# Optimization experiments

Measured on AMD Instinct MI355X. Metric: run time of the kernel, lower is better.

Reference implementation:

```python
import jax, jax.numpy as jnp
import numpy as np

N_RNA, N_PROT, D, C, E = 20000, 5000, 128, 4, 500000

def setup_inputs() -> dict:
    key = jax.random.key(0)
    k1, k2, k3, k4, k5, k6 = jax.random.split(key, 6)
    return {
        "RNA_inputs": jax.random.normal(k1, (N_RNA, D), dtype=jnp.float32),
        "protein_inputs": jax.random.normal(k2, (N_PROT, D), dtype=jnp.float32),
        "RNA_indices": jax.random.randint(k3, (E,), 0, N_RNA, dtype=jnp.int64),
        "protein_indices": jax.random.randint(k4, (E,), 0, N_PROT, dtype=jnp.int64),
        "w_relation": jax.random.normal(k5, (C, D), dtype=jnp.float32),
        "weight_classifier": jax.random.normal(k6, (C, C), dtype=jnp.float32),
    }

def reference(RNA_inputs, protein_inputs, RNA_indices, protein_indices, w_relation, weight_classifier):
    # Gather node features for each pair (dropout p=0.0 -> identity)
    r = RNA_inputs[RNA_indices]        # [E, D]
    p = protein_inputs[protein_indices]  # [E, D]
    # Per-class bilinear: basis[e, c] = sum_d r[e,d] * w_relation[c,d] * p[e,d]
    basis = jnp.einsum('ed,cd->ec', r * p, w_relation)  # [E, C]
    # Classifier matmul + ReLU activation
    return jax.nn.relu(basis @ weight_classifier)  # [E, C]
```

## Files before the change

kernel.cpp:

```cpp
#include <hip/hip_runtime.h>

#define DIM 128
#define NCLS 4

typedef _Float16 f16x4 __attribute__((ext_vector_type(4)));
typedef _Float16 f16x8 __attribute__((ext_vector_type(8)));

__global__ __launch_bounds__(256) void cvt_both_kernel(
    const float* __restrict__ s1, _Float16* __restrict__ d1, int n1,
    const float* __restrict__ s2, _Float16* __restrict__ d2, int n2)
{
    const int total = n1 + n2;
    int i = (blockIdx.x * blockDim.x + threadIdx.x) * 8;
    const int stride = gridDim.x * blockDim.x * 8;
    for (; i < total; i += stride) {
        const float* s; _Float16* d; int j;
        if (i < n1) { s = s1; d = d1; j = i; }
        else        { s = s2; d = d2; j = i - n1; }
        const float4 a = *(const float4*)(s + j);
        const float4 b = *(const float4*)(s + j + 4);
        f16x8 o;
        o[0] = (_Float16)a.x; o[1] = (_Float16)a.y;
        o[2] = (_Float16)a.z; o[3] = (_Float16)a.w;
        o[4] = (_Float16)b.x; o[5] = (_Float16)b.y;
        o[6] = (_Float16)b.z; o[7] = (_Float16)b.w;
        *(f16x8*)(d + j) = o;
    }
}

__device__ __forceinline__ float reduce4(float b0, float b1, float b2, float b3, int lane)
{
    const bool lo1 = (lane & 1) == 0;
    float k0 = lo1 ? b0 : b2, s0 = lo1 ? b2 : b0;
    float k1 = lo1 ? b1 : b3, s1 = lo1 ? b3 : b1;
    float v0 = k0 + __shfl_xor(s0, 1, 32);
    float v1 = k1 + __shfl_xor(s1, 1, 32);
    const bool lo2 = (lane & 2) == 0;
    float k = lo2 ? v0 : v1, s = lo2 ? v1 : v0;
    float v = k + __shfl_xor(s, 2, 32);
    v += __shfl_xor(v, 4, 32);
    v += __shfl_xor(v, 8, 32);
    v += __shfl_xor(v, 16, 32);
    return v;
}

__device__ __forceinline__ void dot_store(
    f16x4 r, f16x4 p, const float4& wf0, const float4& wf1,
    const float4& wf2, const float4& wf3, int lane, int cls,
    float* __restrict__ out, long e)
{
    const f16x4 q = r * p;
    const float qx = (float)q[0], qy = (float)q[1];
    const float qz = (float)q[2], qw = (float)q[3];
    float b0 = qx * wf0.x + qy * wf0.y + qz * wf0.z + qw * wf0.w;
    float b1 = qx * wf1.x + qy * wf1.y + qz * wf1.z + qw * wf1.w;
    float b2 = qx * wf2.x + qy * wf2.y + qz * wf2.z + qw * wf2.w;
    float b3 = qx * wf3.x + qy * wf3.y + qz * wf3.z + qw * wf3.w;
    const float v = reduce4(b0, b1, b2, b3, lane);
    if (lane < 4) out[e * NCLS + cls] = fmaxf(v, 0.0f);
}

__global__ __launch_bounds__(256, 5) void decoder_ilp8_kernel(
    const _Float16* __restrict__ rna,
    const _Float16* __restrict__ prot,
    const int*   __restrict__ ridx,
    const int*   __restrict__ pidx,
    const float* __restrict__ wrel,
    const float* __restrict__ wcls,
    float*       __restrict__ out,
    int nEdges)
{
    const int l32 = threadIdx.x & 31;
    const int hw  = (blockIdx.x * blockDim.x + threadIdx.x) >> 5;
    const int nhw = (gridDim.x * blockDim.x) >> 5;

    const float4 w0 = *(const float4*)(wrel + 0 * DIM + l32 * 4);
    const float4 w1 = *(const float4*)(wrel + 1 * DIM + l32 * 4);
    const float4 w2 = *(const float4*)(wrel + 2 * DIM + l32 * 4);
    const float4 w3 = *(const float4*)(wrel + 3 * DIM + l32 * 4);
    float wc[16];
#pragma unroll
    for (int i = 0; i < 16; ++i) wc[i] = wcls[i];
    float4 wf0, wf1, wf2, wf3;
    {
        float4* wfp[4] = {&wf0, &wf1, &wf2, &wf3};
#pragma unroll
        for (int j = 0; j < 4; ++j) {
            wfp[j]->x = wc[j] * w0.x + wc[4 + j] * w1.x + wc[8 + j] * w2.x + wc[12 + j] * w3.x;
            wfp[j]->y = wc[j] * w0.y + wc[4 + j] * w1.y + wc[8 + j] * w2.y + wc[12 + j] * w3.y;
            wfp[j]->z = wc[j] * w0.z + wc[4 + j] * w1.z + wc[8 + j] * w2.z + wc[12 + j] * w3.z;
            wfp[j]->w = wc[j] * w0.w + wc[4 + j] * w1.w + wc[8 + j] * w2.w + wc[12 + j] * w3.w;
        }
    }
    const int cls = ((l32 & 1) << 1) | ((l32 >> 1) & 1);

    const long step = (long)nhw * 8;
    long e0 = (long)hw * 8;
    if (e0 + 7 >= nEdges) return;

    int4 riA = *(const int4*)(ridx + e0);
    int4 piA = *(const int4*)(pidx + e0);
    int4 riB = *(const int4*)(ridx + e0 + 4);
    int4 piB = *(const int4*)(pidx + e0 + 4);

    for (;;) {
        const f16x4 rA0 = ((const f16x4*)(rna + (size_t)riA.x * DIM))[l32];
        const f16x4 rA1 = ((const f16x4*)(rna + (size_t)riA.y * DIM))[l32];
        const f16x4 rA2 = ((const f16x4*)(rna + (size_t)riA.z * DIM))[l32];
        const f16x4 rA3 = ((const f16x4*)(rna + (size_t)riA.w * DIM))[l32];
        const f16x4 pA0 = ((const f16x4*)(prot + (size_t)piA.x * DIM))[l32];
        const f16x4 pA1 = ((const f16x4*)(prot + (size_t)piA.y * DIM))[l32];
        const f16x4 pA2 = ((const f16x4*)(prot + (size_t)piA.z * DIM))[l32];
        const f16x4 pA3 = ((const f16x4*)(prot + (size_t)piA.w * DIM))[l32];
        const f16x4 rB0 = ((const f16x4*)(rna + (size_t)riB.x * DIM))[l32];
        const f16x4 rB1 = ((const f16x4*)(rna + (size_t)riB.y * DIM))[l32];
        const f16x4 rB2 = ((const f16x4*)(rna + (size_t)riB.z * DIM))[l32];
        const f16x4 rB3 = ((const f16x4*)(rna + (size_t)riB.w * DIM))[l32];
        const f16x4 pB0 = ((const f16x4*)(prot + (size_t)piB.x * DIM))[l32];
        const f16x4 pB1 = ((const f16x4*)(prot + (size_t)piB.y * DIM))[l32];
        const f16x4 pB2 = ((const f16x4*)(prot + (size_t)piB.z * DIM))[l32];
        const f16x4 pB3 = ((const f16x4*)(prot + (size_t)piB.w * DIM))[l32];

        const long en = e0 + step;
        const bool more = (en + 7) < nEdges;
        if (more) {
            riA = *(const int4*)(ridx + en);
            piA = *(const int4*)(pidx + en);
            riB = *(const int4*)(ridx + en + 4);
            piB = *(const int4*)(pidx + en + 4);
        }

        dot_store(rA0, pA0, wf0, wf1, wf2, wf3, l32, cls, out, e0 + 0);
        dot_store(rA1, pA1, wf0, wf1, wf2, wf3, l32, cls, out, e0 + 1);
        dot_store(rA2, pA2, wf0, wf1, wf2, wf3, l32, cls, out, e0 + 2);
        dot_store(rA3, pA3, wf0, wf1, wf2, wf3, l32, cls, out, e0 + 3);
        dot_store(rB0, pB0, wf0, wf1, wf2, wf3, l32, cls, out, e0 + 4);
        dot_store(rB1, pB1, wf0, wf1, wf2, wf3, l32, cls, out, e0 + 5);
        dot_store(rB2, pB2, wf0, wf1, wf2, wf3, l32, cls, out, e0 + 6);
        dot_store(rB3, pB3, wf0, wf1, wf2, wf3, l32, cls, out, e0 + 7);

        if (!more) break;
        e0 = en;
    }
}

__global__ __launch_bounds__(256) void decoder_f32_kernel(
    const float* __restrict__ rna, const float* __restrict__ prot,
    const int* __restrict__ ridx, const int* __restrict__ pidx,
    const float* __restrict__ wrel, const float* __restrict__ wcls,
    float* __restrict__ out, int nEdges)
{
    const int lane32 = threadIdx.x & 31;
    const int hw     = (blockIdx.x * blockDim.x + threadIdx.x) >> 5;
    const int nhw    = (gridDim.x * blockDim.x) >> 5;
    const float4 w0 = *(const float4*)(wrel + 0 * DIM + lane32 * 4);
    const float4 w1 = *(const float4*)(wrel + 1 * DIM + lane32 * 4);
    const float4 w2 = *(const float4*)(wrel + 2 * DIM + lane32 * 4);
    const float4 w3 = *(const float4*)(wrel + 3 * DIM + lane32 * 4);
    float wc[16];
#pragma unroll
    for (int i = 0; i < 16; ++i) wc[i] = wcls[i];
    float4 wf[4];
#pragma unroll
    for (int j = 0; j < 4; ++j) {
        wf[j].x = wc[j] * w0.x + wc[4 + j] * w1.x + wc[8 + j] * w2.x + wc[12 + j] * w3.x;
        wf[j].y = wc[j] * w0.y + wc[4 + j] * w1.y + wc[8 + j] * w2.y + wc[12 + j] * w3.y;
        wf[j].z = wc[j] * w0.z + wc[4 + j] * w1.z + wc[8 + j] * w2.z + wc[12 + j] * w3.z;
        wf[j].w = wc[j] * w0.w + wc[4 + j] * w1.w + wc[8 + j] * w2.w + wc[12 + j] * w3.w;
    }
    const int cls   = ((lane32 & 1) << 1) | ((lane32 >> 1) & 1);
    const int lelem = lane32 * 4;
    for (int e = hw; e < nEdges; e += nhw) {
        const float4 r = *(const float4*)(rna  + (size_t)ridx[e] * DIM + lelem);
        const float4 p = *(const float4*)(prot + (size_t)pidx[e] * DIM + lelem);
        float qx = r.x * p.x, qy = r.y * p.y, qz = r.z * p.z, qw = r.w * p.w;
        float b0 = qx * wf[0].x + qy * wf[0].y + qz * wf[0].z + qw * wf[0].w;
        float b1 = qx * wf[1].x + qy * wf[1].y + qz * wf[1].z + qw * wf[1].w;
        float b2 = qx * wf[2].x + qy * wf[2].y + qz * wf[2].z + qw * wf[2].w;
        float b3 = qx * wf[3].x + qy * wf[3].y + qz * wf[3].z + qw * wf[3].w;
        const float v = reduce4(b0, b1, b2, b3, lane32);
        if (lane32 < 4) out[(size_t)e * NCLS + cls] = fmaxf(v, 0.0f);
    }
}

extern "C" void kernel_launch(void* const* d_in, const int* in_sizes, int n_in,
                              void* d_out, int out_size, void* d_ws, size_t ws_size,
                              hipStream_t stream) {
    const float* rna  = (const float*)d_in[0];
    const float* prot = (const float*)d_in[1];
    const int*   ridx = (const int*)d_in[2];
    const int*   pidx = (const int*)d_in[3];
    const float* wrel = (const float*)d_in[4];
    const float* wcls = (const float*)d_in[5];
    float*       out  = (float*)d_out;

    const int nRnaElems  = in_sizes[0];
    const int nProtElems = in_sizes[1];
    const int nEdges     = in_sizes[2];

    const size_t rnaBytes  = (size_t)nRnaElems * 2;
    const size_t needBytes = rnaBytes + (size_t)nProtElems * 2;

    if (ws_size >= needBytes && (nEdges % 8) == 0 && nEdges >= 8 &&
        (nRnaElems % 8) == 0 && (nProtElems % 8) == 0) {
        _Float16* rnaH  = (_Float16*)d_ws;
        _Float16* protH = (_Float16*)((char*)d_ws + rnaBytes);

        const int totalElems = nRnaElems + nProtElems;
        const int cvtBlocks  = (totalElems / 8 + 255) / 256;
        hipLaunchKernelGGL(cvt_both_kernel, dim3(cvtBlocks), dim3(256), 0, stream,
                           rna, rnaH, nRnaElems, prot, protH, nProtElems);

        hipLaunchKernelGGL(decoder_ilp8_kernel, dim3(2048), dim3(256), 0, stream,
                           rnaH, protH, ridx, pidx, wrel, wcls, out, nEdges);
    } else {
        hipLaunchKernelGGL(decoder_f32_kernel, dim3(8192), dim3(256), 0, stream,
                           rna, prot, ridx, pidx, wrel, wcls, out, nEdges);
    }
}
```

Before: 105.2 us.

## Raise per-halfwave ILP to 12 edges and use fp16 dot2 for class projections

Each 32-lane group now gathers 12 edges per iteration instead of 8, using clamped overlapping groups of 4 to handle tails. The per-edge class dot products use packed fp16 dot2 instructions, with the combined weights kept in fp16. The occupancy hint drops from 5 to 4 to make room for the extra registers. The aim is more memory-level parallelism on the random gathers and fewer ALU ops, at the cost of lower occupancy, some redundant tail writes and reduced weight precision.

```diff
diff --git a/kernel.cpp b/kernel.cpp
--- a/kernel.cpp
+++ b/kernel.cpp
@@ -3,6 +3,7 @@
 #define DIM 128
 #define NCLS 4
 
+typedef _Float16 f16x2 __attribute__((ext_vector_type(2)));
 typedef _Float16 f16x4 __attribute__((ext_vector_type(4)));
 typedef _Float16 f16x8 __attribute__((ext_vector_type(8)));
 
@@ -45,22 +46,21 @@
 }
 
 __device__ __forceinline__ void dot_store(
-    f16x4 r, f16x4 p, const float4& wf0, const float4& wf1,
-    const float4& wf2, const float4& wf3, int lane, int cls,
-    float* __restrict__ out, long e)
+    f16x4 r, f16x4 p, const f16x2 (&wl)[4], const f16x2 (&wh)[4],
+    int lane, int cls, float* __restrict__ out, int e)
 {
     const f16x4 q = r * p;
-    const float qx = (float)q[0], qy = (float)q[1];
-    const float qz = (float)q[2], qw = (float)q[3];
-    float b0 = qx * wf0.x + qy * wf0.y + qz * wf0.z + qw * wf0.w;
-    float b1 = qx * wf1.x + qy * wf1.y + qz * wf1.z + qw * wf1.w;
-    float b2 = qx * wf2.x + qy * wf2.y + qz * wf2.z + qw * wf2.w;
-    float b3 = qx * wf3.x + qy * wf3.y + qz * wf3.z + qw * wf3.w;
+    const f16x2 ql = {q[0], q[1]};
+    const f16x2 qh = {q[2], q[3]};
+    const float b0 = __builtin_amdgcn_fdot2(ql, wl[0], __builtin_amdgcn_fdot2(qh, wh[0], 0.0f, false), false);
+    const float b1 = __builtin_amdgcn_fdot2(ql, wl[1], __builtin_amdgcn_fdot2(qh, wh[1], 0.0f, false), false);
+    const float b2 = __builtin_amdgcn_fdot2(ql, wl[2], __builtin_amdgcn_fdot2(qh, wh[2], 0.0f, false), false);
+    const float b3 = __builtin_amdgcn_fdot2(ql, wl[3], __builtin_amdgcn_fdot2(qh, wh[3], 0.0f, false), false);
     const float v = reduce4(b0, b1, b2, b3, lane);
-    if (lane < 4) out[e * NCLS + cls] = fmaxf(v, 0.0f);
-}
-
-__global__ __launch_bounds__(256, 5) void decoder_ilp8_kernel(
+    if (lane < 4) out[(size_t)e * NCLS + cls] = fmaxf(v, 0.0f);
+}
+
+__global__ __launch_bounds__(256, 4) void decoder_ilp12_kernel(
     const _Float16* __restrict__ rna,
     const _Float16* __restrict__ prot,
     const int*   __restrict__ ridx,
@@ -81,66 +81,90 @@
     float wc[16];
 #pragma unroll
     for (int i = 0; i < 16; ++i) wc[i] = wcls[i];
-    float4 wf0, wf1, wf2, wf3;
-    {
-        float4* wfp[4] = {&wf0, &wf1, &wf2, &wf3};
-#pragma unroll
-        for (int j = 0; j < 4; ++j) {
-            wfp[j]->x = wc[j] * w0.x + wc[4 + j] * w1.x + wc[8 + j] * w2.x + wc[12 + j] * w3.x;
-            wfp[j]->y = wc[j] * w0.y + wc[4 + j] * w1.y + wc[8 + j] * w2.y + wc[12 + j] * w3.y;
-            wfp[j]->z = wc[j] * w0.z + wc[4 + j] * w1.z + wc[8 + j] * w2.z + wc[12 + j] * w3.z;
-            wfp[j]->w = wc[j] * w0.w + wc[4 + j] * w1.w + wc[8 + j] * w2.w + wc[12 + j] * w3.w;
+    f16x2 wl[4], wh[4];
+#pragma unroll
+    for (int j = 0; j < 4; ++j) {
+        const float x = wc[j] * w0.x + wc[4 + j] * w1.x + wc[8 + j] * w2.x + wc[12 + j] * w3.x;
+        const float y = wc[j] * w0.y + wc[4 + j] * w1.y + wc[8 + j] * w2.y + wc[12 + j] * w3.y;
+        const float z = wc[j] * w0.z + wc[4 + j] * w1.z + wc[8 + j] * w2.z + wc[12 + j] * w3.z;
+        const float w = wc[j] * w0.w + wc[4 + j] * w1.w + wc[8 + j] * w2.w + wc[12 + j] * w3.w;
+        wl[j][0] = (_Float16)x; wl[j][1] = (_Float16)y;
+        wh[j][0] = (_Float16)z; wh[j][1] = (_Float16)w;
+    }
+    const int cls = ((l32 & 1) << 1) | ((l32 >> 1) & 1);
+
+    const long step = (long)nhw * 12;
+    long e0 = (long)hw * 12;
+    if (e0 >= nEdges) return;
+
+    int gb0 = (e0 + 3  >= nEdges) ? nEdges - 4 : (int)e0;
+    int gb1 = (e0 + 7  >= nEdges) ? nEdges - 4 : (int)(e0 + 4);
+    int gb2 = (e0 + 11 >= nEdges) ? nEdges - 4 : (int)(e0 + 8);
+
+    int4 ri0 = *(const int4*)(ridx + gb0);
+    int4 pi0 = *(const int4*)(pidx + gb0);
+    int4 ri1 = *(const int4*)(ridx + gb1);
+    int4 pi1 = *(const int4*)(pidx + gb1);
+    int4 ri2 = *(const int4*)(ridx + gb2);
+    int4 pi2 = *(const int4*)(pidx + gb2);
+
+    for (;;) {
+        const f16x4 rA0 = ((const f16x4*)(rna + (size_t)ri0.x * DIM))[l32];
+        const f16x4 rA1 = ((const f16x4*)(rna + (size_t)ri0.y * DIM))[l32];
+        const f16x4 rA2 = ((const f16x4*)(rna + (size_t)ri0.z * DIM))[l32];
+        const f16x4 rA3 = ((const f16x4*)(rna + (size_t)ri0.w * DIM))[l32];
+        const f16x4 pA0 = ((const f16x4*)(prot + (size_t)pi0.x * DIM))[l32];
+        const f16x4 pA1 = ((const f16x4*)(prot + (size_t)pi0.y * DIM))[l32];
+        const f16x4 pA2 = ((const f16x4*)(prot + (size_t)pi0.z * DIM))[l32];
+        const f16x4 pA3 = ((const f16x4*)(prot + (size_t)pi0.w * DIM))[l32];
+        const f16x4 rB0 = ((const f16x4*)(rna + (size_t)ri1.x * DIM))[l32];
+        const f16x4 rB1 = ((const f16x4*)(rna + (size_t)ri1.y * DIM))[l32];
+        const f16x4 rB2 = ((const f16x4*)(rna + (size_t)ri1.z * DIM))[l32];
+        const f16x4 rB3 = ((const f16x4*)(rna + (size_t)ri1.w * DIM))[l32];
+        const f16x4 pB0 = ((const f16x4*)(prot + (size_t)pi1.x * DIM))[l32];
+        const f16x4 pB1 = ((const f16x4*)(prot + (size_t)pi1.y * DIM))[l32];
+        const f16x4 pB2 = ((const f16x4*)(prot + (size_t)pi1.z * DIM))[l32];
+        const f16x4 pB3 = ((const f16x4*)(prot + (size_t)pi1.w * DIM))[l32];
+        const f16x4 rC0 = ((const f16x4*)(rna + (size_t)ri2.x * DIM))[l32];
+        const f16x4 rC1 = ((const f16x4*)(rna + (size_t)ri2.y * DIM))[l32];
+        const f16x4 rC2 = ((const f16x4*)(rna + (size_t)ri2.z * DIM))[l32];
+        const f16x4 rC3 = ((const f16x4*)(rna + (size_t)ri2.w * DIM))[l32];
+        const f16x4 pC0 = ((const f16x4*)(prot + (size_t)pi2.x * DIM))[l32];
+        const f16x4 pC1 = ((const f16x4*)(prot + (size_t)pi2.y * DIM))[l32];
+        const f16x4 pC2 = ((const f16x4*)(prot + (size_t)pi2.z * DIM))[l32];
+        const f16x4 pC3 = ((const f16x4*)(prot + (size_t)pi2.w * DIM))[l32];
+
+        const long en = e0 + step;
+        const bool more = en < nEdges;
+        int ngb0 = gb0, ngb1 = gb1, ngb2 = gb2;
+        if (more) {
+            ngb0 = (en + 3  >= nEdges) ? nEdges - 4 : (int)en;
+            ngb1 = (en + 7  >= nEdges) ? nEdges - 4 : (int)(en + 4);
+            ngb2 = (en + 11 >= nEdges) ? nEdges - 4 : (int)(en + 8);
+            ri0 = *(const int4*)(ridx + ngb0);
+            pi0 = *(const int4*)(pidx + ngb0);
+            ri1 = *(const int4*)(ridx + ngb1);
+            pi1 = *(const int4*)(pidx + ngb1);
+            ri2 = *(const int4*)(ridx + ngb2);
+            pi2 = *(const int4*)(pidx + ngb2);
         }
-    }
-    const int cls = ((l32 & 1) << 1) | ((l32 >> 1) & 1);
-
-    const long step = (long)nhw * 8;
-    long e0 = (long)hw * 8;
-    if (e0 + 7 >= nEdges) return;
-
-    int4 riA = *(const int4*)(ridx + e0);
-    int4 piA = *(const int4*)(pidx + e0);
-    int4 riB = *(const int4*)(ridx + e0 + 4);
-    int4 piB = *(const int4*)(pidx + e0 + 4);
-
-    for (;;) {
-        const f16x4 rA0 = ((const f16x4*)(rna + (size_t)riA.x * DIM))[l32];
-        const f16x4 rA1 = ((const f16x4*)(rna + (size_t)riA.y * DIM))[l32];
-        const f16x4 rA2 = ((const f16x4*)(rna + (size_t)riA.z * DIM))[l32];
-        const f16x4 rA3 = ((const f16x4*)(rna + (size_t)riA.w * DIM))[l32];
-        const f16x4 pA0 = ((const f16x4*)(prot + (size_t)piA.x * DIM))[l32];
-        const f16x4 pA1 = ((const f16x4*)(prot + (size_t)piA.y * DIM))[l32];
-        const f16x4 pA2 = ((const f16x4*)(prot + (size_t)piA.z * DIM))[l32];
-        const f16x4 pA3 = ((const f16x4*)(prot + (size_t)piA.w * DIM))[l32];
-        const f16x4 rB0 = ((const f16x4*)(rna + (size_t)riB.x * DIM))[l32];
-        const f16x4 rB1 = ((const f16x4*)(rna + (size_t)riB.y * DIM))[l32];
-        const f16x4 rB2 = ((const f16x4*)(rna + (size_t)riB.z * DIM))[l32];
-        const f16x4 rB3 = ((const f16x4*)(rna + (size_t)riB.w * DIM))[l32];
-        const f16x4 pB0 = ((const f16x4*)(prot + (size_t)piB.x * DIM))[l32];
-        const f16x4 pB1 = ((const f16x4*)(prot + (size_t)piB.y * DIM))[l32];
-        const f16x4 pB2 = ((const f16x4*)(prot + (size_t)piB.z * DIM))[l32];
-        const f16x4 pB3 = ((const f16x4*)(prot + (size_t)piB.w * DIM))[l32];
-
-        const long en = e0 + step;
-        const bool more = (en + 7) < nEdges;
-        if (more) {
-            riA = *(const int4*)(ridx + en);
-            piA = *(const int4*)(pidx + en);
-            riB = *(const int4*)(ridx + en + 4);
-            piB = *(const int4*)(pidx + en + 4);
-        }
-
-        dot_store(rA0, pA0, wf0, wf1, wf2, wf3, l32, cls, out, e0 + 0);
-        dot_store(rA1, pA1, wf0, wf1, wf2, wf3, l32, cls, out, e0 + 1);
-        dot_store(rA2, pA2, wf0, wf1, wf2, wf3, l32, cls, out, e0 + 2);
-        dot_store(rA3, pA3, wf0, wf1, wf2, wf3, l32, cls, out, e0 + 3);
-        dot_store(rB0, pB0, wf0, wf1, wf2, wf3, l32, cls, out, e0 + 4);
-        dot_store(rB1, pB1, wf0, wf1, wf2, wf3, l32, cls, out, e0 + 5);
-        dot_store(rB2, pB2, wf0, wf1, wf2, wf3, l32, cls, out, e0 + 6);
-        dot_store(rB3, pB3, wf0, wf1, wf2, wf3, l32, cls, out, e0 + 7);
+
+        dot_store(rA0, pA0, wl, wh, l32, cls, out, gb0 + 0);
+        dot_store(rA1, pA1, wl, wh, l32, cls, out, gb0 + 1);
+        dot_store(rA2, pA2, wl, wh, l32, cls, out, gb0 + 2);
+        dot_store(rA3, pA3, wl, wh, l32, cls, out, gb0 + 3);
+        dot_store(rB0, pB0, wl, wh, l32, cls, out, gb1 + 0);
+        dot_store(rB1, pB1, wl, wh, l32, cls, out, gb1 + 1);
+        dot_store(rB2, pB2, wl, wh, l32, cls, out, gb1 + 2);
+        dot_store(rB3, pB3, wl, wh, l32, cls, out, gb1 + 3);
+        dot_store(rC0, pC0, wl, wh, l32, cls, out, gb2 + 0);
+        dot_store(rC1, pC1, wl, wh, l32, cls, out, gb2 + 1);
+        dot_store(rC2, pC2, wl, wh, l32, cls, out, gb2 + 2);
+        dot_store(rC3, pC3, wl, wh, l32, cls, out, gb2 + 3);
 
         if (!more) break;
         e0 = en;
+        gb0 = ngb0; gb1 = ngb1; gb2 = ngb2;
     }
 }
 
@@ -201,7 +225,7 @@
     const size_t rnaBytes  = (size_t)nRnaElems * 2;
     const size_t needBytes = rnaBytes + (size_t)nProtElems * 2;
 
-    if (ws_size >= needBytes && (nEdges % 8) == 0 && nEdges >= 8 &&
+    if (ws_size >= needBytes && nEdges >= 4 &&
         (nRnaElems % 8) == 0 && (nProtElems % 8) == 0) {
         _Float16* rnaH  = (_Float16*)d_ws;
         _Float16* protH = (_Float16*)((char*)d_ws + rnaBytes);
@@ -211,7 +235,7 @@
         hipLaunchKernelGGL(cvt_both_kernel, dim3(cvtBlocks), dim3(256), 0, stream,
                            rna, rnaH, nRnaElems, prot, protH, nProtElems);
 
-        hipLaunchKernelGGL(decoder_ilp8_kernel, dim3(2048), dim3(256), 0, stream,
+        hipLaunchKernelGGL(decoder_ilp12_kernel, dim3(2048), dim3(256), 0, stream,
                            rnaH, protH, ridx, pidx, wrel, wcls, out, nEdges);
     } else {
         hipLaunchKernelGGL(decoder_f32_kernel, dim3(8192), dim3(256), 0, stream,
```

After: 106.8 us. About the same (+1.5%).
